# Kernel tuning notes

Measured on AMD Instinct MI355X. Metric: run time of the kernel, lower is better.

Reference implementation:

```python
import jax, jax.numpy as jnp
import numpy as np

LN_EPS = 1e-5

def _layer_norm(x, g, b):
    mu = jnp.mean(x, axis=-1, keepdims=True)
    var = jnp.mean(jnp.square(x - mu), axis=-1, keepdims=True)
    return (x - mu) * jax.lax.rsqrt(var + LN_EPS) * g + b

def setup_inputs() -> dict:
    key = jax.random.key(0)
    ks = jax.random.split(key, 12)
    B, L, E, H, W = 4, 1024, 1024, 16, 128
    s = 0.02
    return {
        "x": jax.random.normal(ks[0], (B, L, E), dtype=jnp.float32),
        "in_proj_w": jax.random.normal(ks[1], (3 * E, E), dtype=jnp.float32) * s,
        "in_proj_b": jnp.zeros((3 * E,), dtype=jnp.float32),
        "out_proj_w": jax.random.normal(ks[2], (E, E), dtype=jnp.float32) * s,
        "out_proj_b": jnp.zeros((E,), dtype=jnp.float32),
        "ln1_g": jnp.ones((E,), dtype=jnp.float32),
        "ln1_b": jnp.zeros((E,), dtype=jnp.float32),
        "w1": jax.random.normal(ks[3], (4 * E, E), dtype=jnp.float32) * s,
        "b1": jnp.zeros((4 * E,), dtype=jnp.float32),
        "w2": jax.random.normal(ks[4], (E, 4 * E), dtype=jnp.float32) * s,
        "b2": jnp.zeros((E,), dtype=jnp.float32),
        "ln2_g": jnp.ones((E,), dtype=jnp.float32),
        "ln2_b": jnp.zeros((E,), dtype=jnp.float32),
        "n_head": 16,
        "window_size": 128,
    }

def reference(x, in_proj_w, in_proj_b, out_proj_w, out_proj_b,
              ln1_g, ln1_b, w1, b1, w2, b2, ln2_g, ln2_b,
              n_head, window_size):
    B, L, E = x.shape
    H = n_head
    D = E // H
    # qkv projection (torch Linear convention: y = x @ W.T + b)
    qkv = jnp.einsum('ble,fe->blf', x, in_proj_w) + in_proj_b  # [B,L,3E]
    q, k, v = jnp.split(qkv, 3, axis=-1)
    q = q.reshape(B, L, H, D).transpose(0, 2, 1, 3)  # [B,H,L,D]
    k = k.reshape(B, L, H, D).transpose(0, 2, 1, 3)
    v = v.reshape(B, L, H, D).transpose(0, 2, 1, 3)
    scores = jnp.einsum('bhld,bhmd->bhlm', q, k) / np.sqrt(D)  # [B,H,L,L]
    # banded window mask: allowed iff |i-j| <= window_size (same as the double loop)
    idx = jnp.arange(L)
    band = jnp.abs(idx[:, None] - idx[None, :]) <= window_size  # [L,L]
    scores = jnp.where(band[None, None], scores, -jnp.inf)
    attn = jax.nn.softmax(scores, axis=-1)  # [B,H,L,L]
    ctx = jnp.einsum('bhlm,bhmd->bhld', attn, v)  # [B,H,L,D]
    ctx = ctx.transpose(0, 2, 1, 3).reshape(B, L, E)
    attn_out = jnp.einsum('ble,fe->blf', ctx, out_proj_w) + out_proj_b
    attn_weights = jnp.mean(attn, axis=1)  # torch MHA averages heads -> [B,L,L]
    # residual + norm1 (dropout is identity in eval)
    h = _layer_norm(x + attn_out, ln1_g, ln1_b)
    # positionwise FFN
    ff = jnp.einsum('ble,fe->blf', h, w1) + b1
    ff = jax.nn.relu(ff)
    ff = jnp.einsum('blf,ef->ble', ff, w2) + b2
    out = _layer_norm(h + ff, ln2_g, ln2_b)
    return (out, attn_weights)
```

## Files before the change

### kernel.cpp

```cpp
#include <hip/hip_runtime.h>

#define BB 4
#define LL 1024
#define EE 1024
#define HH 16
#define DD 64

typedef __attribute__((ext_vector_type(8))) short short8;
typedef __attribute__((ext_vector_type(4))) float floatx4;

#define PSTR ((size_t)4096 * 1024)

__device__ __forceinline__ float bf2f(short s) {
    union { unsigned u; float f; } c;
    c.u = ((unsigned)(unsigned short)s) << 16;
    return c.f;
}
__device__ __forceinline__ short f2bf(float f) {
    union { float f; unsigned u; } c; c.f = f;
    unsigned r = c.u + 0x7fffu + ((c.u >> 16) & 1u);
    return (short)(r >> 16);
}

__device__ __forceinline__ void async_copy16(const void* g, void* l) {
    __builtin_amdgcn_global_load_lds(
        (const __attribute__((address_space(1))) unsigned int*)g,
        (__attribute__((address_space(3))) unsigned int*)l, 16, 0, 0);
}

__global__ __launch_bounds__(256) void cvt5(
    const float* __restrict__ x, const float* __restrict__ wqkv,
    const float* __restrict__ wo, const float* __restrict__ w1,
    const float* __restrict__ w2,
    short* __restrict__ xb, short* __restrict__ wqkvb, short* __restrict__ wob,
    short* __restrict__ w1b, short* __restrict__ w2b)
{
    int bi = blockIdx.x;
    const float* in; short* out; int base;
    if      (bi <  4096) { in = x;    out = xb;    base = 0;     }
    else if (bi <  7168) { in = wqkv; out = wqkvb; base = 4096;  }
    else if (bi <  8192) { in = wo;   out = wob;   base = 7168;  }
    else if (bi < 12288) { in = w1;   out = w1b;   base = 8192;  }
    else                 { in = w2;   out = w2b;   base = 12288; }
    int i = (bi - base) * 256 + threadIdx.x;
    float4 v = ((const float4*)in)[i];
    unsigned long long u =
          (unsigned long long)(unsigned short)f2bf(v.x)
        | ((unsigned long long)(unsigned short)f2bf(v.y) << 16)
        | ((unsigned long long)(unsigned short)f2bf(v.z) << 32)
        | ((unsigned long long)(unsigned short)f2bf(v.w) << 48);
    ((unsigned long long*)out)[i] = u;
}

template<bool RELU, bool WVT, bool SK>
__global__ __launch_bounds__(256) void gemm_bt(
    const short* __restrict__ A, const short* __restrict__ Bw,
    const float* __restrict__ bias,
    short* __restrict__ Cb, short* __restrict__ VTp,
    int M, int N, int K, int Ksp)
{
    __shared__ union U {
        struct { short As[128 * 64]; short Bs[128 * 64]; } s;
        short Cs[128 * 136];
    } u;
    const int tid  = threadIdx.x;
    const int wave = tid >> 6, lane = tid & 63;
    const int m0 = blockIdx.x * 128, n0 = blockIdx.y * 128;
    const int wm = (wave & 1) * 64, wn = (wave >> 1) * 64;
    const int kbase = SK ? blockIdx.z * Ksp : 0;

    floatx4 acc[4][4];
#pragma unroll
    for (int i = 0; i < 4; ++i)
#pragma unroll
        for (int j = 0; j < 4; ++j) acc[i][j] = (floatx4){0.f, 0.f, 0.f, 0.f};

    const int srow = wave * 8 + (lane >> 3);
    const int scol = (((lane & 7) ^ ((lane >> 3) & 7))) * 8;
    const short* gA = A  + (size_t)(m0 + srow) * K + kbase + scol;
    const short* gB = Bw + (size_t)(n0 + srow) * K + kbase + scol;
    short* lA = u.s.As + wave * 512;
    short* lB = u.s.Bs + wave * 512;

    const int fr = lane & 15, quad = lane >> 4;
    const int kiters = (SK ? Ksp : K) >> 6;
    for (int kt = 0; kt < kiters; ++kt) {
#pragma unroll
        for (int s = 0; s < 4; ++s) {
            async_copy16(gA + (size_t)s * 32 * K, lA + s * 2048);
            async_copy16(gB + (size_t)s * 32 * K, lB + s * 2048);
        }
        gA += 64; gB += 64;
        __syncthreads();
#pragma unroll
        for (int ks = 0; ks < 2; ++ks) {
            short8 af[4], bf[4];
#pragma unroll
            for (int i = 0; i < 4; ++i) {
                int pos = ((ks * 4 + quad) ^ (fr & 7)) * 8;
                af[i] = *(const short8*)&u.s.As[(wm + i * 16 + fr) * 64 + pos];
                bf[i] = *(const short8*)&u.s.Bs[(wn + i * 16 + fr) * 64 + pos];
            }
#pragma unroll
            for (int i = 0; i < 4; ++i)
#pragma unroll
                for (int j = 0; j < 4; ++j)
                    acc[i][j] = __builtin_amdgcn_mfma_f32_16x16x32_bf16(af[i], bf[j], acc[i][j], 0, 0, 0);
        }
        __syncthreads();
    }

    const int cc = lane & 15;
    const int rb = (lane >> 4) * 4;
#pragma unroll
    for (int j = 0; j < 4; ++j) {
        int col = wn + j * 16 + cc;
        float bv = SK ? 0.0f : bias[n0 + col];
#pragma unroll
        for (int i = 0; i < 4; ++i) {
            int row = wm + i * 16 + rb;
#pragma unroll
            for (int r = 0; r < 4; ++r) {
                float v = acc[i][j][r] + bv;
                if (RELU) v = fmaxf(v, 0.0f);
                u.Cs[(row + r) * 136 + col] = f2bf(v);
            }
        }
    }
    __syncthreads();
    short* Co = Cb + (SK ? (size_t)blockIdx.z * PSTR : 0);
    const int trow = tid >> 4, tcol = (tid & 15) * 8;
#pragma unroll
    for (int p = 0; p < 8; ++p) {
        int row = p * 16 + trow;
        short8 vv = *(const short8*)&u.Cs[row * 136 + tcol];
        *(short8*)&Co[(size_t)(m0 + row) * N + n0 + tcol] = vv;
        if (WVT) {
            int gc0 = n0 + tcol;
            if (gc0 >= 2048) {
                int tok = m0 + row;
                int hc = (gc0 - 2048) >> 6, d0 = (gc0 - 2048) & 63;
                short* vrow = VTp + ((size_t)((tok >> 10) * 16 + hc) * 64 + d0) * 1024 + (tok & 1023);
#pragma unroll
                for (int e = 0; e < 8; ++e) vrow[(size_t)e * 1024] = vv[e];
            }
        }
    }
}

__global__ __launch_bounds__(256) void ln_kernel(
    const float* __restrict__ xa, const short* __restrict__ parts, int nparts,
    const float* __restrict__ bias,
    const float* __restrict__ g, const float* __restrict__ beta,
    float* __restrict__ outf, short* __restrict__ outb)
{
    const int row = blockIdx.x;
    const int tid = threadIdx.x;
    float4 va = ((const float4*)(xa + (size_t)row * EE))[tid];
    float4 vb = ((const float4*)bias)[tid];
    float v0 = va.x + vb.x, v1 = va.y + vb.y, v2 = va.z + vb.z, v3 = va.w + vb.w;
#pragma unroll 4
    for (int p = 0; p < nparts; ++p) {
        unsigned long long u8 = ((const unsigned long long*)(parts + p * PSTR + (size_t)row * EE))[tid];
        v0 += bf2f((short)(u8 & 0xffff));
        v1 += bf2f((short)((u8 >> 16) & 0xffff));
        v2 += bf2f((short)((u8 >> 32) & 0xffff));
        v3 += bf2f((short)(u8 >> 48));
    }
    float s  = v0 + v1 + v2 + v3;
    float ss = v0 * v0 + v1 * v1 + v2 * v2 + v3 * v3;
#pragma unroll
    for (int o = 1; o < 64; o <<= 1) { s += __shfl_xor(s, o); ss += __shfl_xor(ss, o); }
    __shared__ float red[8];
    if ((tid & 63) == 0) { red[(tid >> 6) * 2] = s; red[(tid >> 6) * 2 + 1] = ss; }
    __syncthreads();
    s  = red[0] + red[2] + red[4] + red[6];
    ss = red[1] + red[3] + red[5] + red[7];
    float mean = s * (1.0f / EE);
    float var  = ss * (1.0f / EE) - mean * mean;
    float rstd = rsqrtf(var + 1e-5f);
    float4 vg = ((const float4*)g)[tid];
    float4 vt = ((const float4*)beta)[tid];
    float o0 = (v0 - mean) * rstd * vg.x + vt.x;
    float o1 = (v1 - mean) * rstd * vg.y + vt.y;
    float o2 = (v2 - mean) * rstd * vg.z + vt.z;
    float o3 = (v3 - mean) * rstd * vg.w + vt.w;
    if (outf) ((float4*)(outf + (size_t)row * EE))[tid] = make_float4(o0, o1, o2, o3);
    if (outb) {
        unsigned long long u =
              (unsigned long long)(unsigned short)f2bf(o0)
            | ((unsigned long long)(unsigned short)f2bf(o1) << 16)
            | ((unsigned long long)(unsigned short)f2bf(o2) << 32)
            | ((unsigned long long)(unsigned short)f2bf(o3) << 48);
        ((unsigned long long*)(outb + (size_t)row * EE))[tid] = u;
    }
}

__global__ __launch_bounds__(256) void attn_mfma(
    const short* __restrict__ qkv,
    const short* __restrict__ vt,
    short* __restrict__ ctxp,
    short* __restrict__ pb)
{
    __shared__ float Sb[32 * 324];
    __shared__ short Pl[32 * 322];
    const int tid = threadIdx.x, wave = tid >> 6, lane = tid & 63;
    const int quad = lane >> 4, mcol = lane & 15;
    const int i0 = blockIdx.x * 32, h = blockIdx.y, b = blockIdx.z;
    const int jb0 = i0 - 128;

    const short* qb = qkv + (size_t)(b * 1024) * 3072 + h * 64;
    const short* kb = qb + 1024;

    short8 aq[2][2];
#pragma unroll
    for (int mt = 0; mt < 2; ++mt)
#pragma unroll
        for (int ks = 0; ks < 2; ++ks)
            aq[mt][ks] = *(const short8*)(qb + (size_t)(i0 + mt * 16 + mcol) * 3072 + ks * 32 + quad * 8);

    floatx4 sacc[2][5];
#pragma unroll
    for (int mt = 0; mt < 2; ++mt)
#pragma unroll
        for (int c = 0; c < 5; ++c) sacc[mt][c] = (floatx4){0.f, 0.f, 0.f, 0.f};

#pragma unroll
    for (int c = 0; c < 5; ++c) {
        int ct = c * 4 + wave;
        int j = jb0 + ct * 16 + mcol;
        j = min(max(j, 0), 1023);
        const short* kr = kb + (size_t)j * 3072 + quad * 8;
        short8 b0 = *(const short8*)kr;
        short8 b1 = *(const short8*)(kr + 32);
        sacc[0][c] = __builtin_amdgcn_mfma_f32_16x16x32_bf16(aq[0][0], b0, sacc[0][c], 0, 0, 0);
        sacc[1][c] = __builtin_amdgcn_mfma_f32_16x16x32_bf16(aq[1][0], b0, sacc[1][c], 0, 0, 0);
        sacc[0][c] = __builtin_amdgcn_mfma_f32_16x16x32_bf16(aq[0][1], b1, sacc[0][c], 0, 0, 0);
        sacc[1][c] = __builtin_amdgcn_mfma_f32_16x16x32_bf16(aq[1][1], b1, sacc[1][c], 0, 0, 0);
    }
#pragma unroll
    for (int mt = 0; mt < 2; ++mt)
#pragma unroll
        for (int c = 0; c < 5; ++c) {
            int jo = (c * 4 + wave) * 16 + mcol;
            int rowb = mt * 16 + quad * 4;
#pragma unroll
            for (int r = 0; r < 4; ++r)
                Sb[(rowb + r) * 324 + jo] = sacc[mt][c][r];
        }
    __syncthreads();

    for (int rr = 0; rr < 8; ++rr) {
        const int r = wave * 8 + rr;
        float sv[5];
#pragma unroll
        for (int t = 0; t < 5; ++t) {
            int jo = lane + t * 64;
            bool val = (jo >= r) && (jo <= r + 256) && ((unsigned)(jb0 + jo) < 1024u);
            sv[t] = val ? Sb[r * 324 + jo] * 0.125f : -1e30f;
        }
        float m = sv[0];
#pragma unroll
        for (int t = 1; t < 5; ++t) m = fmaxf(m, sv[t]);
#pragma unroll
        for (int o = 32; o; o >>= 1) m = fmaxf(m, __shfl_xor(m, o));
        float l = 0.f, p[5];
#pragma unroll
        for (int t = 0; t < 5; ++t) { p[t] = __expf(sv[t] - m); l += p[t]; }
#pragma unroll
        for (int o = 32; o; o >>= 1) l += __shfl_xor(l, o);
        float inv = 1.0f / l;
        short* pbrow = pb + ((size_t)(b * 1024 + i0 + r) * 16 + h) * 272;
#pragma unroll
        for (int t = 0; t < 5; ++t) {
            int jo = lane + t * 64;
            short pv = f2bf(p[t] * inv);
            Pl[r * 322 + jo] = pv;
            int jr = jo - r;
            if ((unsigned)jr < 272u) pbrow[jr] = pv;
        }
    }
    __syncthreads();

    const int mt = wave & 1, dt0 = (wave >> 1) * 2;
    floatx4 cacc[2];
    cacc[0] = (floatx4){0.f, 0.f, 0.f, 0.f};
    cacc[1] = (floatx4){0.f, 0.f, 0.f, 0.f};
    const short* vtb = vt + (size_t)((b * 16 + h) * 64) * 1024;
#pragma unroll
    for (int jc = 0; jc < 10; ++jc) {
        short8 ap = *(const short8*)&Pl[(mt * 16 + mcol) * 322 + jc * 32 + quad * 8];
        int jg = jb0 + jc * 32 + quad * 8;
        if ((unsigned)jg >= 1024u) jg = 0;
#pragma unroll
        for (int e = 0; e < 2; ++e) {
            short8 bv = *(const short8*)(vtb + (size_t)((dt0 + e) * 16 + mcol) * 1024 + jg);
            cacc[e] = __builtin_amdgcn_mfma_f32_16x16x32_bf16(ap, bv, cacc[e], 0, 0, 0);
        }
    }
#pragma unroll
    for (int e = 0; e < 2; ++e) {
        int col = h * 64 + (dt0 + e) * 16 + mcol;
#pragma unroll
        for (int r = 0; r < 4; ++r) {
            int row = i0 + mt * 16 + quad * 4 + r;
            ctxp[(size_t)(b * 1024 + row) * 1024 + col] = f2bf(cacc[e][r]);
        }
    }
}

__global__ __launch_bounds__(256) void pb_reduce(const short* __restrict__ pb,
                                                 float* __restrict__ aw)
{
    const int i = blockIdx.x & 1023, b = blockIdx.x >> 10;
    __shared__ short P[16 * 272];
    const unsigned* src = (const unsigned*)(pb + (size_t)(b * 1024 + i) * 16 * 272);
    for (int t = threadIdx.x; t < 16 * 272 / 2; t += 256)
        ((unsigned*)P)[t] = src[t];
    __syncthreads();
    float* row = aw + ((size_t)(b * 1024) + i) * 1024;
    for (int j = threadIdx.x; j < 1024; j += 256) {
        int jr = j - i + 128;
        float s = 0.f;
        if ((unsigned)jr < 272u) {
#pragma unroll
            for (int hh = 0; hh < 16; ++hh)
                s += bf2f(P[hh * 272 + jr]);
            s *= (1.0f / 16.0f);
        }
        row[j] = s;
    }
}

extern "C" void kernel_launch(void* const* d_in, const int* in_sizes, int n_in,
                              void* d_out, int out_size, void* d_ws, size_t ws_size,
                              hipStream_t stream) {
    const float* x    = (const float*)d_in[0];
    const float* wqkv = (const float*)d_in[1];
    const float* bqkv = (const float*)d_in[2];
    const float* wo   = (const float*)d_in[3];
    const float* bo   = (const float*)d_in[4];
    const float* g1   = (const float*)d_in[5];
    const float* be1  = (const float*)d_in[6];
    const float* w1   = (const float*)d_in[7];
    const float* bb1  = (const float*)d_in[8];
    const float* w2   = (const float*)d_in[9];
    const float* bb2  = (const float*)d_in[10];
    const float* g2   = (const float*)d_in[11];
    const float* be2  = (const float*)d_in[12];

    char* ws = (char*)d_ws;
    size_t off = 0;
    auto take = [&](size_t bytes) {
        void* p = ws + off;
        off += (bytes + 255) & ~(size_t)255;
        return p;
    };
    short* xb     = (short*)take((size_t)4096 * 1024 * 2);
    short* wqkv_b = (short*)take((size_t)3072 * 1024 * 2);
    short* wo_b   = (short*)take((size_t)1024 * 1024 * 2);
    short* w1_b   = (short*)take((size_t)4096 * 1024 * 2);
    short* w2_b   = (short*)take((size_t)1024 * 4096 * 2);
    short* qkv_b  = (short*)take((size_t)4096 * 3072 * 2);
    short* ctx_b  = (short*)take((size_t)4096 * 1024 * 2);
    short* ff2_p  = qkv_b;
    short* attn_p = (short*)take((size_t)2 * 4096 * 1024 * 2);
    float* h_f    = (float*)take((size_t)4096 * 1024 * 4);
    short* vt_ws  = (short*)h_f;
    short* h_b    = (short*)take((size_t)4096 * 1024 * 2);
    short* pb_ws  = (short*)take((size_t)4 * 1024 * 16 * 272 * 2);
    short* ff_b   = pb_ws;

    float* out_f = (float*)d_out;
    float* attnW = (float*)d_out + (size_t)4 * 1024 * 1024;

    cvt5<<<16384, 256, 0, stream>>>(x, wqkv, wo, w1, w2, xb, wqkv_b, wo_b, w1_b, w2_b);

    gemm_bt<false, true, false><<<dim3(32, 24), 256, 0, stream>>>(
        xb, wqkv_b, bqkv, qkv_b, vt_ws, 4096, 3072, 1024, 1024);

    attn_mfma<<<dim3(32, 16, 4), 256, 0, stream>>>(qkv_b, vt_ws, ctx_b, pb_ws);

    pb_reduce<<<4096, 256, 0, stream>>>(pb_ws, attnW);

    gemm_bt<false, false, true><<<dim3(32, 8, 2), 256, 0, stream>>>(
        ctx_b, wo_b, nullptr, attn_p, nullptr, 4096, 1024, 1024, 512);

    ln_kernel<<<4096, 256, 0, stream>>>(x, attn_p, 2, bo, g1, be1, h_f, h_b);

    gemm_bt<true, false, false><<<dim3(32, 32), 256, 0, stream>>>(
        h_b, w1_b, bb1, ff_b, nullptr, 4096, 4096, 1024, 1024);

    gemm_bt<false, false, true><<<dim3(32, 8, 4), 256, 0, stream>>>(
        ff_b, w2_b, nullptr, ff2_p, nullptr, 4096, 1024, 4096, 1024);

    ln_kernel<<<4096, 256, 0, stream>>>(h_f, ff2_p, 4, bb2, g2, be2, out_f, nullptr);
}
```

Measured before the change: 377.2 us.

## Restructure attention kernel: register softmax, 512 threads, swizzled LDS, head-major grid

The attention kernel now runs 8 waves per block. Each wave computes one 16-row by 80-column score slice and keeps it in registers, so the float score staging buffer in shared memory goes away. The row max and row sum are combined across the four column-quarter waves with a small shared reduction array and two barriers. The P tile in LDS uses an XOR swizzle to avoid bank conflicts, and the 1D grid is ordered so the 16 heads of a batch and row block are adjacent, which should help L2 reuse of K and V. In exchange it adds extra barriers and cross-wave reductions.

Result: no change. 375.5 us (-0.5%).

```diff
diff --git a/kernel.cpp b/kernel.cpp
--- a/kernel.cpp
+++ b/kernel.cpp
@@ -196,116 +196,115 @@
     }
 }
 
-__global__ __launch_bounds__(256) void attn_mfma(
+__global__ __launch_bounds__(512, 8) void attn_mfma(
     const short* __restrict__ qkv,
     const short* __restrict__ vt,
     short* __restrict__ ctxp,
     short* __restrict__ pb)
 {
-    __shared__ float Sb[32 * 324];
-    __shared__ short Pl[32 * 322];
+    __shared__ short Pl[32 * 320];
+    __shared__ float Red[4][2][32];
     const int tid = threadIdx.x, wave = tid >> 6, lane = tid & 63;
     const int quad = lane >> 4, mcol = lane & 15;
-    const int i0 = blockIdx.x * 32, h = blockIdx.y, b = blockIdx.z;
+    const int id = blockIdx.x;
+    const int i0 = (id >> 6) * 32, h = id & 15, b = (id >> 4) & 3;
     const int jb0 = i0 - 128;
 
     const short* qb = qkv + (size_t)(b * 1024) * 3072 + h * 64;
     const short* kb = qb + 1024;
 
-    short8 aq[2][2];
-#pragma unroll
-    for (int mt = 0; mt < 2; ++mt)
-#pragma unroll
-        for (int ks = 0; ks < 2; ++ks)
-            aq[mt][ks] = *(const short8*)(qb + (size_t)(i0 + mt * 16 + mcol) * 3072 + ks * 32 + quad * 8);
-
-    floatx4 sacc[2][5];
-#pragma unroll
-    for (int mt = 0; mt < 2; ++mt)
-#pragma unroll
-        for (int c = 0; c < 5; ++c) sacc[mt][c] = (floatx4){0.f, 0.f, 0.f, 0.f};
-
+    const int mt = wave >> 2, qtr = wave & 3;
+    const short* qrow = qb + (size_t)(i0 + mt * 16 + mcol) * 3072 + quad * 8;
+    short8 aq0 = *(const short8*)qrow;
+    short8 aq1 = *(const short8*)(qrow + 32);
+
+    floatx4 sacc[5];
+#pragma unroll
+    for (int c = 0; c < 5; ++c) sacc[c] = (floatx4){0.f, 0.f, 0.f, 0.f};
 #pragma unroll
     for (int c = 0; c < 5; ++c) {
-        int ct = c * 4 + wave;
-        int j = jb0 + ct * 16 + mcol;
+        int j = jb0 + (qtr * 5 + c) * 16 + mcol;
         j = min(max(j, 0), 1023);
         const short* kr = kb + (size_t)j * 3072 + quad * 8;
         short8 b0 = *(const short8*)kr;
         short8 b1 = *(const short8*)(kr + 32);
-        sacc[0][c] = __builtin_amdgcn_mfma_f32_16x16x32_bf16(aq[0][0], b0, sacc[0][c], 0, 0, 0);
-        sacc[1][c] = __builtin_amdgcn_mfma_f32_16x16x32_bf16(aq[1][0], b0, sacc[1][c], 0, 0, 0);
-        sacc[0][c] = __builtin_amdgcn_mfma_f32_16x16x32_bf16(aq[0][1], b1, sacc[0][c], 0, 0, 0);
-        sacc[1][c] = __builtin_amdgcn_mfma_f32_16x16x32_bf16(aq[1][1], b1, sacc[1][c], 0, 0, 0);
-    }
-#pragma unroll
-    for (int mt = 0; mt < 2; ++mt)
+        sacc[c] = __builtin_amdgcn_mfma_f32_16x16x32_bf16(aq0, b0, sacc[c], 0, 0, 0);
+        sacc[c] = __builtin_amdgcn_mfma_f32_16x16x32_bf16(aq1, b1, sacc[c], 0, 0, 0);
+    }
+
+    const int row0 = mt * 16 + quad * 4;
+#pragma unroll
+    for (int r = 0; r < 4; ++r) {
+        int row = row0 + r;
+        float m = -1e30f;
 #pragma unroll
         for (int c = 0; c < 5; ++c) {
-            int jo = (c * 4 + wave) * 16 + mcol;
-            int rowb = mt * 16 + quad * 4;
-#pragma unroll
-            for (int r = 0; r < 4; ++r)
-                Sb[(rowb + r) * 324 + jo] = sacc[mt][c][r];
-        }
-    __syncthreads();
-
-    for (int rr = 0; rr < 8; ++rr) {
-        const int r = wave * 8 + rr;
-        float sv[5];
-#pragma unroll
-        for (int t = 0; t < 5; ++t) {
-            int jo = lane + t * 64;
-            bool val = (jo >= r) && (jo <= r + 256) && ((unsigned)(jb0 + jo) < 1024u);
-            sv[t] = val ? Sb[r * 324 + jo] * 0.125f : -1e30f;
-        }
-        float m = sv[0];
-#pragma unroll
-        for (int t = 1; t < 5; ++t) m = fmaxf(m, sv[t]);
-#pragma unroll
-        for (int o = 32; o; o >>= 1) m = fmaxf(m, __shfl_xor(m, o));
-        float l = 0.f, p[5];
-#pragma unroll
-        for (int t = 0; t < 5; ++t) { p[t] = __expf(sv[t] - m); l += p[t]; }
-#pragma unroll
-        for (int o = 32; o; o >>= 1) l += __shfl_xor(l, o);
-        float inv = 1.0f / l;
-        short* pbrow = pb + ((size_t)(b * 1024 + i0 + r) * 16 + h) * 272;
-#pragma unroll
-        for (int t = 0; t < 5; ++t) {
-            int jo = lane + t * 64;
-            short pv = f2bf(p[t] * inv);
-            Pl[r * 322 + jo] = pv;
-            int jr = jo - r;
+            int jo = (qtr * 5 + c) * 16 + mcol;
+            bool val = (jo >= row) && (jo <= row + 256) && ((unsigned)(jb0 + jo) < 1024u);
+            float s = val ? sacc[c][r] * 0.125f : -1e30f;
+            sacc[c][r] = s;
+            m = fmaxf(m, s);
+        }
+        m = fmaxf(m, __shfl_xor(m, 1));
+        m = fmaxf(m, __shfl_xor(m, 2));
+        m = fmaxf(m, __shfl_xor(m, 4));
+        m = fmaxf(m, __shfl_xor(m, 8));
+        if (mcol == 0) Red[qtr][0][row] = m;
+    }
+    __syncthreads();
+#pragma unroll
+    for (int r = 0; r < 4; ++r) {
+        int row = row0 + r;
+        float M = fmaxf(fmaxf(Red[0][0][row], Red[1][0][row]),
+                        fmaxf(Red[2][0][row], Red[3][0][row]));
+        float l = 0.f;
+#pragma unroll
+        for (int c = 0; c < 5; ++c) {
+            float p = __expf(sacc[c][r] - M);
+            sacc[c][r] = p;
+            l += p;
+        }
+        l += __shfl_xor(l, 1);
+        l += __shfl_xor(l, 2);
+        l += __shfl_xor(l, 4);
+        l += __shfl_xor(l, 8);
+        if (mcol == 0) Red[qtr][1][row] = l;
+    }
+    __syncthreads();
+#pragma unroll
+    for (int r = 0; r < 4; ++r) {
+        int row = row0 + r;
+        float inv = 1.0f / (Red[0][1][row] + Red[1][1][row] +
+                            Red[2][1][row] + Red[3][1][row]);
+        short* pbrow = pb + ((size_t)(b * 1024 + i0 + row) * 16 + h) * 272;
+#pragma unroll
+        for (int c = 0; c < 5; ++c) {
+            int jo = (qtr * 5 + c) * 16 + mcol;
+            short pv = f2bf(sacc[c][r] * inv);
+            Pl[row * 320 + (((jo >> 3) ^ (row & 7)) * 8) + (jo & 7)] = pv;
+            int jr = jo - row;
             if ((unsigned)jr < 272u) pbrow[jr] = pv;
         }
     }
     __syncthreads();
 
-    const int mt = wave & 1, dt0 = (wave >> 1) * 2;
-    floatx4 cacc[2];
-    cacc[0] = (floatx4){0.f, 0.f, 0.f, 0.f};
-    cacc[1] = (floatx4){0.f, 0.f, 0.f, 0.f};
-    const short* vtb = vt + (size_t)((b * 16 + h) * 64) * 1024;
+    const int pmt = wave & 1, dt = wave >> 1;
+    floatx4 cacc = (floatx4){0.f, 0.f, 0.f, 0.f};
+    const short* vrow = vt + ((size_t)((b * 16 + h) * 64) + dt * 16 + mcol) * 1024;
+    const int prow = (pmt * 16 + mcol) * 320;
 #pragma unroll
     for (int jc = 0; jc < 10; ++jc) {
-        short8 ap = *(const short8*)&Pl[(mt * 16 + mcol) * 322 + jc * 32 + quad * 8];
+        short8 ap = *(const short8*)&Pl[prow + (((jc * 4 + quad) ^ (mcol & 7)) * 8)];
         int jg = jb0 + jc * 32 + quad * 8;
         if ((unsigned)jg >= 1024u) jg = 0;
-#pragma unroll
-        for (int e = 0; e < 2; ++e) {
-            short8 bv = *(const short8*)(vtb + (size_t)((dt0 + e) * 16 + mcol) * 1024 + jg);
-            cacc[e] = __builtin_amdgcn_mfma_f32_16x16x32_bf16(ap, bv, cacc[e], 0, 0, 0);
-        }
-    }
-#pragma unroll
-    for (int e = 0; e < 2; ++e) {
-        int col = h * 64 + (dt0 + e) * 16 + mcol;
-#pragma unroll
-        for (int r = 0; r < 4; ++r) {
-            int row = i0 + mt * 16 + quad * 4 + r;
-            ctxp[(size_t)(b * 1024 + row) * 1024 + col] = f2bf(cacc[e][r]);
-        }
+        short8 bv = *(const short8*)(vrow + jg);
+        cacc = __builtin_amdgcn_mfma_f32_16x16x32_bf16(ap, bv, cacc, 0, 0, 0);
+    }
+    int col = h * 64 + dt * 16 + mcol;
+#pragma unroll
+    for (int r = 0; r < 4; ++r) {
+        int row = i0 + pmt * 16 + quad * 4 + r;
+        ctxp[(size_t)(b * 1024 + row) * 1024 + col] = f2bf(cacc[r]);
     }
 }
 
@@ -379,7 +378,7 @@
     gemm_bt<false, true, false><<<dim3(32, 24), 256, 0, stream>>>(
         xb, wqkv_b, bqkv, qkv_b, vt_ws, 4096, 3072, 1024, 1024);
 
-    attn_mfma<<<dim3(32, 16, 4), 256, 0, stream>>>(qkv_b, vt_ws, ctx_b, pb_ws);
+    attn_mfma<<<2048, 512, 0, stream>>>(qkv_b, vt_ws, ctx_b, pb_ws);
 
     pb_reduce<<<4096, 256, 0, stream>>>(pb_ws, attnW);
 
```
